# Performance work log

Measured on AMD Instinct MI355X. Metric: run time of the kernel, lower is better.

## Reference

```python
import jax, jax.numpy as jnp
import numpy as np

B, N, IN_F = 8, 1024, 128
H, FH = 4, 32
NEG_SLOPE = 0.2


def setup_inputs() -> dict:
    key = jax.random.key(0)
    k_x, k_adj, k_w, k_a = jax.random.split(key, 4)
    x = jax.random.normal(k_x, (B, N, IN_F), dtype=jnp.float32)
    adj_raw = jax.random.uniform(k_adj, (B, N, N), dtype=jnp.float32)
    adj = jnp.where(adj_raw < 0.5, 0.0, adj_raw)
    # nn.Linear(in, out*H, bias=False): weight shape [H*FH, IN_F]
    W_weight = jax.random.normal(k_w, (H * FH, IN_F), dtype=jnp.float32) * 0.1
    # attn param: [H, 2*FH + 1] (use_edge_feat=True)
    attn = jax.random.normal(k_a, (H, 2 * FH + 1), dtype=jnp.float32) * 0.1
    return {"x": x, "adj": adj, "W_weight": W_weight, "attn": attn}


def reference(x, adj, W_weight, attn):
    # h = W(x): [B, N, H, FH]
    h = jnp.einsum("bni,oi->bno", x, W_weight).reshape(B, N, H, FH)
    # decompose a^T [h_i || h_j || A_ij] = a_src.h_i + a_dst.h_j + a_e*A_ij
    a_src = attn[:, :FH]            # [H, FH]
    a_dst = attn[:, FH:2 * FH]      # [H, FH]
    a_e = attn[:, 2 * FH]           # [H]
    src = jnp.einsum("bnhf,hf->bnh", h, a_src)   # score for node as i
    dst = jnp.einsum("bnhf,hf->bnh", h, a_dst)   # score for node as j
    # e[b,i,j,h]
    e = src[:, :, None, :] + dst[:, None, :, :] + adj[..., None] * a_e
    e = jnp.where(e >= 0, e, NEG_SLOPE * e)      # LeakyReLU
    no_edge = (adj == 0.0)[..., None]            # [B, N, N, 1]
    e = jnp.where(no_edge, -jnp.inf, e)
    alpha = jax.nn.softmax(e, axis=2)            # softmax over j
    alpha = jnp.nan_to_num(alpha, nan=0.0)
    # dropout: eval mode -> identity
    # out[b,i,h,f] = sum_j alpha[b,i,j,h] * h[b,j,h,f]
    out = jnp.einsum("bijh,bjhf->bihf", alpha, h).reshape(B, N, H * FH)
    return out, alpha
```

## Files before the change

### kernel.cpp

```cpp
#include <hip/hip_runtime.h>

#define NEG 0.2f
constexpr int B_ = 8, N_ = 1024;

__global__ __launch_bounds__(256) void gat_h_kernel(
    const float* __restrict__ x, const float* __restrict__ Ww,
    const float* __restrict__ attn,
    float* __restrict__ hfeat, float* __restrict__ srcv, float* __restrict__ dstv)
{
    __shared__ float Wl[128 * 128];
    const int tid = threadIdx.x;
    const int row0 = blockIdx.x * 16;

    #pragma unroll
    for (int k = 0; k < 16; ++k) {
        int f = tid + k * 256;
        int o = f >> 5, ib = f & 31;
        float4 w = *(const float4*)(Ww + o * 128 + ib * 4);
        *(float4*)&Wl[o * 128 + ((ib ^ ((o >> 2) & 7)) << 2)] = w;
    }
    __syncthreads();

    const int colg = tid & 31;
    const int rg   = tid >> 5;
    const int swz  = colg & 7;
    float acc[2][4] = {};
    const float* xr = x + (size_t)(row0 + rg * 2) * 128;

    #pragma unroll 8
    for (int is = 0; is < 32; ++is) {
        float4 x0 = *(const float4*)(xr + is * 4);
        float4 x1 = *(const float4*)(xr + 128 + is * 4);
        #pragma unroll
        for (int cc = 0; cc < 4; ++cc) {
            float4 wv = *(const float4*)&Wl[(colg * 4 + cc) * 128 + ((is ^ swz) << 2)];
            acc[0][cc] = fmaf(x0.x, wv.x, acc[0][cc]);
            acc[0][cc] = fmaf(x0.y, wv.y, acc[0][cc]);
            acc[0][cc] = fmaf(x0.z, wv.z, acc[0][cc]);
            acc[0][cc] = fmaf(x0.w, wv.w, acc[0][cc]);
            acc[1][cc] = fmaf(x1.x, wv.x, acc[1][cc]);
            acc[1][cc] = fmaf(x1.y, wv.y, acc[1][cc]);
            acc[1][cc] = fmaf(x1.z, wv.z, acc[1][cc]);
            acc[1][cc] = fmaf(x1.w, wv.w, acc[1][cc]);
        }
    }
    #pragma unroll
    for (int r = 0; r < 2; ++r) {
        float4 hv = make_float4(acc[r][0], acc[r][1], acc[r][2], acc[r][3]);
        *(float4*)(hfeat + (size_t)(row0 + rg * 2 + r) * 128 + colg * 4) = hv;
    }
    const int hh = colg >> 3;
    float ps[2] = {0.f, 0.f}, pd[2] = {0.f, 0.f};
    #pragma unroll
    for (int cc = 0; cc < 4; ++cc) {
        int fi = (colg & 7) * 4 + cc;
        float as = attn[hh * 65 + fi];
        float ad = attn[hh * 65 + 32 + fi];
        ps[0] = fmaf(acc[0][cc], as, ps[0]); ps[1] = fmaf(acc[1][cc], as, ps[1]);
        pd[0] = fmaf(acc[0][cc], ad, pd[0]); pd[1] = fmaf(acc[1][cc], ad, pd[1]);
    }
    #pragma unroll
    for (int m = 1; m <= 4; m <<= 1) {
        ps[0] += __shfl_xor(ps[0], m); ps[1] += __shfl_xor(ps[1], m);
        pd[0] += __shfl_xor(pd[0], m); pd[1] += __shfl_xor(pd[1], m);
    }
    if ((tid & 7) == 0) {
        #pragma unroll
        for (int r = 0; r < 2; ++r) {
            srcv[(size_t)(row0 + rg * 2 + r) * 4 + hh] = ps[r];
            dstv[(size_t)(row0 + rg * 2 + r) * 4 + hh] = pd[r];
        }
    }
}

__global__ __launch_bounds__(512, 4) void gat_attn_kernel(
    const float* __restrict__ adj, const float* __restrict__ attn,
    const float* __restrict__ hfeat, const float* __restrict__ srcv,
    const float* __restrict__ dstv,
    float* __restrict__ out, float* __restrict__ alpha)
{
    __shared__ float src_l[64];
    __shared__ float rs_l[64];
    __shared__ float adj_t[16 * 68];
    __shared__ float al_l[4 * 64 * 20];
    __shared__ float h_t[64 * 128];

    const int tid  = threadIdx.x;
    const int lane = tid & 63;
    const int w    = tid >> 6;
    const int b    = blockIdx.x >> 6;
    const int i0   = (blockIdx.x & 63) * 16;

    float aE[4];
    #pragma unroll
    for (int h = 0; h < 4; ++h) aE[h] = attn[h * 65 + 64];

    if (tid < 64) src_l[tid] = srcv[(size_t)(b * N_ + i0) * 4 + tid];
    __syncthreads();

    const float* dstb = dstv + (size_t)b * N_ * 4;
    #pragma unroll
    for (int rr = 0; rr < 2; ++rr) {
        int row = w * 2 + rr;
        const float* arow = adj + ((size_t)(b * N_ + i0 + row)) * N_;
        float sd[4];
        #pragma unroll
        for (int h = 0; h < 4; ++h) sd[h] = src_l[row * 4 + h];
        float s[4] = {0.f, 0.f, 0.f, 0.f};
        #pragma unroll
        for (int k = 0; k < 4; ++k) {
            float4 av4 = *(const float4*)(arow + lane * 4 + k * 256);
            const float* avp = (const float*)&av4;
            #pragma unroll
            for (int q = 0; q < 4; ++q) {
                float av = avp[q];
                if (av != 0.f) {
                    int j = lane * 4 + k * 256 + q;
                    float4 dv = *(const float4*)(dstb + j * 4);
                    const float* dvp = (const float*)&dv;
                    #pragma unroll
                    for (int h = 0; h < 4; ++h) {
                        float e = fmaf(av, aE[h], sd[h] + dvp[h]);
                        e = e >= 0.f ? e : NEG * e;
                        s[h] += __expf(e);
                    }
                }
            }
        }
        #pragma unroll
        for (int m = 1; m <= 32; m <<= 1) {
            #pragma unroll
            for (int h = 0; h < 4; ++h) s[h] += __shfl_xor(s[h], m);
        }
        if (lane == 0) {
            #pragma unroll
            for (int h = 0; h < 4; ++h)
                rs_l[row * 4 + h] = s[h] > 0.f ? 1.f / s[h] : 0.f;
        }
    }

    const int rhalf  = w & 1;
    const int hh     = w >> 1;
    const int hf8low = (lane >> 4) & 3;
    const int jc     = lane & 15;
    float4 acc[8][2];
    #pragma unroll
    for (int r = 0; r < 8; ++r) {
        acc[r][0] = make_float4(0.f, 0.f, 0.f, 0.f);
        acc[r][1] = make_float4(0.f, 0.f, 0.f, 0.f);
    }

    for (int jt = 0; jt < 16; ++jt) {
        const int j0 = jt * 64;
        __syncthreads();
        #pragma unroll
        for (int k = 0; k < 4; ++k) {
            int f = tid + k * 512;
            int jj = f >> 5, cb = f & 31;
            float4 hv = *(const float4*)(hfeat + (size_t)(b * N_ + j0 + jj) * 128 + cb * 4);
            *(float4*)&h_t[jj * 128 + ((cb ^ (jj & 7)) << 2)] = hv;
        }
        if (tid < 256) {
            int r = tid >> 4, q = tid & 15;
            float4 av4 = *(const float4*)(adj + ((size_t)(b * N_ + i0 + r)) * N_ + j0 + q * 4);
            *(float4*)&adj_t[r * 68 + q * 4] = av4;
        }
        __syncthreads();
        #pragma unroll
        for (int t = 0; t < 2; ++t) {
            int task = tid + t * 512;
            int r = task & 15, jj = task >> 4;
            float av = adj_t[r * 68 + jj];
            float4 al = make_float4(0.f, 0.f, 0.f, 0.f);
            if (av != 0.f) {
                float4 dv = *(const float4*)(dstb + (j0 + jj) * 4);
                const float* dvp = (const float*)&dv;
                float* alp = (float*)&al;
                #pragma unroll
                for (int h = 0; h < 4; ++h) {
                    float e = fmaf(av, aE[h], src_l[r * 4 + h] + dvp[h]);
                    e = e >= 0.f ? e : NEG * e;
                    alp[h] = __expf(e) * rs_l[r * 4 + h];
                }
            }
            const float* alp = (const float*)&al;
            #pragma unroll
            for (int h = 0; h < 4; ++h)
                al_l[h * 1280 + jj * 20 + r] = alp[h];
            *(float4*)(alpha + ((size_t)(b * N_ + i0 + r) * N_ + j0 + jj) * 4) = al;
        }
        __syncthreads();
        #pragma unroll
        for (int s = 0; s < 4; ++s) {
            int jj = s * 16 + jc;
            float4 aA = *(const float4*)&al_l[hh * 1280 + jj * 20 + rhalf * 8];
            float4 aB = *(const float4*)&al_l[hh * 1280 + jj * 20 + rhalf * 8 + 4];
            int cb0 = hh * 8 + hf8low * 2;
            float4 v0 = *(const float4*)&h_t[jj * 128 + ((cb0 ^ (jj & 7)) << 2)];
            float4 v1 = *(const float4*)&h_t[jj * 128 + (((cb0 + 1) ^ (jj & 7)) << 2)];
#define PVROW(RR, AV)                                                    \
            acc[RR][0].x = fmaf(AV, v0.x, acc[RR][0].x);                 \
            acc[RR][0].y = fmaf(AV, v0.y, acc[RR][0].y);                 \
            acc[RR][0].z = fmaf(AV, v0.z, acc[RR][0].z);                 \
            acc[RR][0].w = fmaf(AV, v0.w, acc[RR][0].w);                 \
            acc[RR][1].x = fmaf(AV, v1.x, acc[RR][1].x);                 \
            acc[RR][1].y = fmaf(AV, v1.y, acc[RR][1].y);                 \
            acc[RR][1].z = fmaf(AV, v1.z, acc[RR][1].z);                 \
            acc[RR][1].w = fmaf(AV, v1.w, acc[RR][1].w);
            PVROW(0, aA.x) PVROW(1, aA.y) PVROW(2, aA.z) PVROW(3, aA.w)
            PVROW(4, aB.x) PVROW(5, aB.y) PVROW(6, aB.z) PVROW(7, aB.w)
#undef PVROW
        }
    }

    #pragma unroll
    for (int m = 1; m <= 8; m <<= 1) {
        #pragma unroll
        for (int r = 0; r < 8; ++r) {
            #pragma unroll
            for (int c = 0; c < 2; ++c) {
                acc[r][c].x += __shfl_xor(acc[r][c].x, m);
                acc[r][c].y += __shfl_xor(acc[r][c].y, m);
                acc[r][c].z += __shfl_xor(acc[r][c].z, m);
                acc[r][c].w += __shfl_xor(acc[r][c].w, m);
            }
        }
    }
    #pragma unroll
    for (int r = 0; r < 8; ++r) {
        #pragma unroll
        for (int c = 0; c < 2; ++c) {
            if ((jc >> 1) == r && (jc & 1) == c) {
                int orow = i0 + rhalf * 8 + r;
                int ocol = hh * 32 + hf8low * 8 + c * 4;
                *(float4*)(out + (size_t)(b * N_ + orow) * 128 + ocol) = acc[r][c];
            }
        }
    }
}

extern "C" void kernel_launch(void* const* d_in, const int* in_sizes, int n_in,
                              void* d_out, int out_size, void* d_ws, size_t ws_size,
                              hipStream_t stream) {
    const float* x    = (const float*)d_in[0];
    const float* adj  = (const float*)d_in[1];
    const float* Ww   = (const float*)d_in[2];
    const float* attn = (const float*)d_in[3];

    float* out   = (float*)d_out;
    float* alpha = out + (size_t)B_ * N_ * 128;

    float* hfeat = (float*)d_ws;
    float* srcv  = hfeat + (size_t)B_ * N_ * 128;
    float* dstv  = srcv + (size_t)B_ * N_ * 4;

    gat_h_kernel<<<512, 256, 0, stream>>>(x, Ww, attn, hfeat, srcv, dstv);
    gat_attn_kernel<<<512, 512, 0, stream>>>(adj, attn, hfeat, srcv, dstv, out, alpha);
}
```

Before: 320.0 us.

## Read adj directly per-lane, drop adj staging tile and its barrier, remap blocks

```diff
diff --git a/kernel.cpp b/kernel.cpp
--- a/kernel.cpp
+++ b/kernel.cpp
@@ -81,15 +81,14 @@
 {
     __shared__ float src_l[64];
     __shared__ float rs_l[64];
-    __shared__ float adj_t[16 * 68];
-    __shared__ float al_l[4 * 64 * 20];
+    __shared__ float al_l[4 * 64 * 21];
     __shared__ float h_t[64 * 128];
 
     const int tid  = threadIdx.x;
     const int lane = tid & 63;
     const int w    = tid >> 6;
-    const int b    = blockIdx.x >> 6;
-    const int i0   = (blockIdx.x & 63) * 16;
+    const int b    = blockIdx.x & 7;
+    const int i0   = (blockIdx.x >> 3) * 16;
 
     float aE[4];
     #pragma unroll
@@ -160,20 +159,13 @@
             float4 hv = *(const float4*)(hfeat + (size_t)(b * N_ + j0 + jj) * 128 + cb * 4);
             *(float4*)&h_t[jj * 128 + ((cb ^ (jj & 7)) << 2)] = hv;
         }
-        if (tid < 256) {
-            int r = tid >> 4, q = tid & 15;
-            float4 av4 = *(const float4*)(adj + ((size_t)(b * N_ + i0 + r)) * N_ + j0 + q * 4);
-            *(float4*)&adj_t[r * 68 + q * 4] = av4;
-        }
-        __syncthreads();
         #pragma unroll
         for (int t = 0; t < 2; ++t) {
-            int task = tid + t * 512;
-            int r = task & 15, jj = task >> 4;
-            float av = adj_t[r * 68 + jj];
+            int r = w + t * 8;
+            float av = adj[((size_t)(b * N_ + i0 + r)) * N_ + j0 + lane];
             float4 al = make_float4(0.f, 0.f, 0.f, 0.f);
             if (av != 0.f) {
-                float4 dv = *(const float4*)(dstb + (j0 + jj) * 4);
+                float4 dv = *(const float4*)(dstb + (j0 + lane) * 4);
                 const float* dvp = (const float*)&dv;
                 float* alp = (float*)&al;
                 #pragma unroll
@@ -186,15 +178,17 @@
             const float* alp = (const float*)&al;
             #pragma unroll
             for (int h = 0; h < 4; ++h)
-                al_l[h * 1280 + jj * 20 + r] = alp[h];
-            *(float4*)(alpha + ((size_t)(b * N_ + i0 + r) * N_ + j0 + jj) * 4) = al;
+                al_l[h * 1344 + lane * 21 + r] = alp[h];
+            *(float4*)(alpha + (((size_t)(b * N_ + i0 + r)) * N_ + j0 + lane) * 4) = al;
         }
         __syncthreads();
         #pragma unroll
         for (int s = 0; s < 4; ++s) {
             int jj = s * 16 + jc;
-            float4 aA = *(const float4*)&al_l[hh * 1280 + jj * 20 + rhalf * 8];
-            float4 aB = *(const float4*)&al_l[hh * 1280 + jj * 20 + rhalf * 8 + 4];
+            const float* ab = &al_l[hh * 1344 + jj * 21 + rhalf * 8];
+            float av8[8];
+            #pragma unroll
+            for (int ri = 0; ri < 8; ++ri) av8[ri] = ab[ri];
             int cb0 = hh * 8 + hf8low * 2;
             float4 v0 = *(const float4*)&h_t[jj * 128 + ((cb0 ^ (jj & 7)) << 2)];
             float4 v1 = *(const float4*)&h_t[jj * 128 + (((cb0 + 1) ^ (jj & 7)) << 2)];
@@ -207,8 +201,8 @@
             acc[RR][1].y = fmaf(AV, v1.y, acc[RR][1].y);                 \
             acc[RR][1].z = fmaf(AV, v1.z, acc[RR][1].z);                 \
             acc[RR][1].w = fmaf(AV, v1.w, acc[RR][1].w);
-            PVROW(0, aA.x) PVROW(1, aA.y) PVROW(2, aA.z) PVROW(3, aA.w)
-            PVROW(4, aB.x) PVROW(5, aB.y) PVROW(6, aB.z) PVROW(7, aB.w)
+            PVROW(0, av8[0]) PVROW(1, av8[1]) PVROW(2, av8[2]) PVROW(3, av8[3])
+            PVROW(4, av8[4]) PVROW(5, av8[5]) PVROW(6, av8[6]) PVROW(7, av8[7])
 #undef PVROW
         }
     }
```

Measured after the change: 279.9 us. 1.14x faster.
